# Kernel tuning notes

Measured on AMD Instinct MI355X. Metric: run time of the kernel, lower is better.

## Reference

```python
import jax, jax.numpy as jnp
import numpy as np

KH, KW = 2, 3          # kernel_size of the masked (shifted) conv
CW = KW // 2           # width padding for order 'A'
B, C, H, W = 8, 32, 256, 256
HID = 64


def _wn(v, g):
    # weight normalization: w = g * v / ||v||, norm over (in, kh, kw) per out channel
    norm = jnp.sqrt(jnp.sum(v * v, axis=(1, 2, 3), keepdims=True))
    return v * (g[:, None, None, None] / norm)


def _conv(x, w, b):
    y = jax.lax.conv_general_dilated(
        x, w, window_strides=(1, 1), padding='VALID',
        dimension_numbers=('NCHW', 'OIHW', 'NCHW'))
    return y + b[None, :, None, None]


def setup_inputs() -> dict:
    key = jax.random.key(0)
    ks = jax.random.split(key, 4)
    x = jax.random.normal(ks[0], (B, C, H, W), dtype=jnp.float32)
    v1 = jax.random.normal(ks[1], (HID, C, KH, KW), dtype=jnp.float32) * 0.05
    g1 = jnp.ones((HID,), dtype=jnp.float32)
    b1 = jnp.zeros((HID,), dtype=jnp.float32)
    v2 = jax.random.normal(ks[2], (2 * C, HID, 1, 1), dtype=jnp.float32) * 0.05
    g2 = jnp.ones((2 * C,), dtype=jnp.float32)
    b2 = jnp.zeros((2 * C,), dtype=jnp.float32)
    return {"x": x, "v1": v1, "g1": g1, "b1": b1, "v2": v2, "g2": g2, "b2": b2}


def reference(x, v1, g1, b1, v2, g2, b2):
    # ShiftedConv2d, order 'A': pad KH rows on top, CW cols each side, drop last
    # row, then VALID conv -> output at row h only sees input rows h-KH..h-1.
    xs = jnp.pad(x, ((0, 0), (0, 0), (KH, 0), (CW, CW)))[:, :, :-1, :]
    h = _conv(xs, _wn(v1, g1), b1)                 # [B, HID, H, W]
    h = jax.nn.elu(h)
    ms = _conv(h, _wn(v2, g2), b2)                 # [B, 2C, H, W]
    mu, log_scale = jnp.split(ms, 2, axis=1)
    scale = jax.nn.sigmoid(log_scale + 2.0)
    out = x * scale + mu                           # affine flow
    logdet = jnp.sum(jnp.log(scale).reshape(x.shape[0], -1), axis=1)  # [B]
    return out, logdet
```

## Files before the change

kernel.cpp:

```cpp
#include <hip/hip_runtime.h>
#include <hip/hip_bf16.h>
#include <math.h>

#define B_   8
#define C_   32
#define H_   256
#define W_   256
#define NPIX (B_*C_*H_*W_)

#define PW    260
#define ROWDW (PW*16)
#define ROWB  (ROWDW*4)

typedef __attribute__((ext_vector_type(8))) short short8;
typedef __attribute__((ext_vector_type(4))) float f32x4;
typedef __attribute__((ext_vector_type(2))) float f32x2;

static __device__ __forceinline__ short f2bf(float f) {
    union { __hip_bfloat16 h; short s; } u; u.h = __float2bfloat16(f); return u.s;
}
static __device__ __forceinline__ int cvtpk(float lo, float hi) {
    int r;
    asm("v_cvt_pk_bf16_f32 %0, %1, %2" : "=v"(r) : "v"(lo), "v"(hi));
    return r;
}

__global__ __launch_bounds__(64) void prep_kernel(
    const float* __restrict__ v1, const float* __restrict__ g1,
    const float* __restrict__ v2, const float* __restrict__ g2,
    short* __restrict__ w1b, short* __restrict__ w2b)
{
    const int t   = threadIdx.x;
    const int bid = blockIdx.x;
    if (bid < 64) {
        const int o = bid;
        float a0 = v1[o*192 + t];
        float a1 = v1[o*192 + t + 64];
        float a2 = v1[o*192 + t + 128];
        float s  = a0*a0 + a1*a1 + a2*a2;
        #pragma unroll
        for (int m = 32; m >= 1; m >>= 1) s += __shfl_xor(s, m, 64);
        const float inv = g1[o] / sqrtf(s);
        const int e0 = t, e1 = t + 64, e2 = t + 128;
        w1b[o*192 + (e0%6)*32 + e0/6] = f2bf(a0*inv);
        w1b[o*192 + (e1%6)*32 + e1/6] = f2bf(a1*inv);
        w1b[o*192 + (e2%6)*32 + e2/6] = f2bf(a2*inv);
    } else {
        const int j = bid - 64;
        float a = v2[j*64 + t];
        float s = a*a;
        #pragma unroll
        for (int m = 32; m >= 1; m >>= 1) s += __shfl_xor(s, m, 64);
        const float inv = g2[j] / sqrtf(s);
        const int mt = t >> 4, r = t & 15;
        const int slot = (mt >> 1)*32 + ((r >> 2) << 3) + ((mt & 1) << 2) + (r & 3);
        w2b[j*64 + slot] = f2bf(a*inv);
    }
}

__global__ __launch_bounds__(256) void flow_kernel(
    const float* __restrict__ x,
    const short* __restrict__ w1b, const short* __restrict__ w2b,
    const float* __restrict__ b1,  const float* __restrict__ b2,
    float* __restrict__ out, float* __restrict__ ldpart)
{
    __shared__ int ldsI[2*ROWDW];

    const int bi0 = blockIdx.x;
    const int bi  = (bi0 & 7) * 256 + (bi0 >> 3);
    const int b   = bi >> 8;
    const int h   = bi & 255;

    const int tid  = threadIdx.x;
    const int l    = tid & 63;
    const int wv   = tid >> 6;
    const int lrow = l & 15;
    const int q    = l >> 4;

    const float* xb = x + (size_t)b * (C_*H_*W_);
    float* ob       = out + (size_t)b * (C_*H_*W_);

    {
        const int r   = tid >> 7;
        const int hr  = h - 2 + r;
        const int u   = tid & 127;
        const int w0  = u << 1;
        const int p0  = w0 + 1, p1 = w0 + 2;
        const int sw0 = (p0 >> 2) & 3, sw1 = (p1 >> 2) & 3;
        if (hr >= 0) {
            const float* pr = xb + (size_t)hr * W_ + w0;
            #pragma unroll
            for (int g = 0; g < 4; ++g) {
                f32x2 a[8];
                #pragma unroll
                for (int j = 0; j < 8; ++j)
                    a[j] = *(const f32x2*)(pr + (size_t)(8*g + j) * (H_*W_));
                int4 d0, d1;
                d0.x = cvtpk(a[0][0], a[1][0]); d0.y = cvtpk(a[2][0], a[3][0]);
                d0.z = cvtpk(a[4][0], a[5][0]); d0.w = cvtpk(a[6][0], a[7][0]);
                d1.x = cvtpk(a[0][1], a[1][1]); d1.y = cvtpk(a[2][1], a[3][1]);
                d1.z = cvtpk(a[4][1], a[5][1]); d1.w = cvtpk(a[6][1], a[7][1]);
                *(int4*)&ldsI[r*ROWDW + p0*16 + ((g ^ sw0) << 2)] = d0;
                *(int4*)&ldsI[r*ROWDW + p1*16 + ((g ^ sw1) << 2)] = d1;
            }
        } else {
            const int4 z4 = {0,0,0,0};
            #pragma unroll
            for (int g = 0; g < 4; ++g) {
                *(int4*)&ldsI[r*ROWDW + p0*16 + ((g ^ sw0) << 2)] = z4;
                *(int4*)&ldsI[r*ROWDW + p1*16 + ((g ^ sw1) << 2)] = z4;
            }
        }
        if (tid < 16) {
            const int rz = tid >> 3;
            const int pz = ((tid >> 2) & 1) ? 257 : 0;
            *(int4*)&ldsI[rz*ROWDW + pz*16 + ((tid & 3) << 2)] = (int4){0,0,0,0};
        }
    }
    __syncthreads();

    f32x4 acc1[4][4];
    #pragma unroll
    for (int mt = 0; mt < 4; ++mt) {
        const f32x4 bv = *(const f32x4*)(b1 + mt*16 + 4*q);
        #pragma unroll
        for (int nt = 0; nt < 4; ++nt) acc1[mt][nt] = bv;
    }

    #pragma unroll
    for (int tap = 0; tap < 6; ++tap) {
        const int rb = (tap < 3) ? 0 : ROWB;
        const int dw = (tap % 3) - 1;
        short8 wf[4];
        #pragma unroll
        for (int mt = 0; mt < 4; ++mt)
            wf[mt] = *(const short8*)(w1b + (mt*16 + lrow)*192 + tap*32 + q*8);
        #pragma unroll
        for (int nt = 0; nt < 4; ++nt) {
            const int p = wv*64 + nt*16 + lrow + dw + 1;
            const int byteoff = rb + p*64 + ((q ^ ((p >> 2) & 3)) << 4);
            const short8 xf = *(const short8*)((const char*)ldsI + byteoff);
            #pragma unroll
            for (int mt = 0; mt < 4; ++mt)
                acc1[mt][nt] = __builtin_amdgcn_mfma_f32_16x16x32_bf16(
                                   wf[mt], xf, acc1[mt][nt], 0, 0, 0);
        }
    }

    #pragma unroll
    for (int mt = 0; mt < 4; ++mt)
        #pragma unroll
        for (int nt = 0; nt < 4; ++nt)
            #pragma unroll
            for (int rg = 0; rg < 4; ++rg) {
                const float v = acc1[mt][nt][rg];
                acc1[mt][nt][rg] = v > 0.f ? v : (__expf(v) - 1.f);
            }

    short8 a2f[2][4];
    #pragma unroll
    for (int kt = 0; kt < 2; ++kt)
        #pragma unroll
        for (int mt2 = 0; mt2 < 4; ++mt2)
            a2f[kt][mt2] = *(const short8*)(w2b + (mt2*16 + lrow)*64 + kt*32 + q*8);

    f32x4 acc2[4][4];
    #pragma unroll
    for (int nt = 0; nt < 4; ++nt) {
        union { int4 i; short8 s; } u0, u1;
        u0.i.x = cvtpk(acc1[0][nt][0], acc1[0][nt][1]);
        u0.i.y = cvtpk(acc1[0][nt][2], acc1[0][nt][3]);
        u0.i.z = cvtpk(acc1[1][nt][0], acc1[1][nt][1]);
        u0.i.w = cvtpk(acc1[1][nt][2], acc1[1][nt][3]);
        u1.i.x = cvtpk(acc1[2][nt][0], acc1[2][nt][1]);
        u1.i.y = cvtpk(acc1[2][nt][2], acc1[2][nt][3]);
        u1.i.z = cvtpk(acc1[3][nt][0], acc1[3][nt][1]);
        u1.i.w = cvtpk(acc1[3][nt][2], acc1[3][nt][3]);
        #pragma unroll
        for (int mt2 = 0; mt2 < 4; ++mt2) {
            f32x4 t0 = __builtin_amdgcn_mfma_f32_16x16x32_bf16(
                           a2f[0][mt2], u0.s, (f32x4){0.f,0.f,0.f,0.f}, 0, 0, 0);
            acc2[mt2][nt] = __builtin_amdgcn_mfma_f32_16x16x32_bf16(
                           a2f[1][mt2], u1.s, t0, 0, 0, 0);
        }
    }

    f32x4 b2m[2], b2s[2];
    #pragma unroll
    for (int mt2 = 0; mt2 < 2; ++mt2) {
        b2m[mt2] = *(const f32x4*)(b2 + mt2*16 + 4*q);
        b2s[mt2] = *(const f32x4*)(b2 + 32 + mt2*16 + 4*q);
    }

    float ldsum = 0.f;
    #pragma unroll
    for (int nt = 0; nt < 4; ++nt) {
        const int px = wv*64 + nt*16 + lrow;
        const int colbase = h*W_ + px;
        float pr8 = 1.f;
        #pragma unroll
        for (int mt2 = 0; mt2 < 2; ++mt2)
            #pragma unroll
            for (int rg = 0; rg < 4; ++rg) {
                const float mu = acc2[mt2][nt][rg]     + b2m[mt2][rg];
                const float z  = acc2[mt2 + 2][nt][rg] + b2s[mt2][rg] + 2.f;
                const float sc = 1.f / (1.f + __expf(-z));
                pr8 *= sc;
                const int j = mt2*16 + 4*q + rg;
                const size_t idx = (size_t)j * (H_*W_) + colbase;
                ob[idx] = xb[idx] * sc + mu;
            }
        ldsum += __logf(pr8);
    }

    #pragma unroll
    for (int m = 32; m >= 1; m >>= 1) ldsum += __shfl_xor(ldsum, m, 64);
    if (l == 0) ldpart[(size_t)bi * 4 + wv] = ldsum;
}

__global__ __launch_bounds__(256) void reduce_kernel(
    const float* __restrict__ ldpart, float* __restrict__ logdet)
{
    __shared__ float r4[4];
    const int b = blockIdx.x;
    const int t = threadIdx.x;
    const f32x4 v = *(const f32x4*)(ldpart + (size_t)b*1024 + t*4);
    float s = v[0] + v[1] + v[2] + v[3];
    #pragma unroll
    for (int m = 32; m >= 1; m >>= 1) s += __shfl_xor(s, m, 64);
    if ((t & 63) == 0) r4[t >> 6] = s;
    __syncthreads();
    if (t == 0) logdet[b] = r4[0] + r4[1] + r4[2] + r4[3];
}

extern "C" void kernel_launch(void* const* d_in, const int* in_sizes, int n_in,
                              void* d_out, int out_size, void* d_ws, size_t ws_size,
                              hipStream_t stream)
{
    const float* x  = (const float*)d_in[0];
    const float* v1 = (const float*)d_in[1];
    const float* g1 = (const float*)d_in[2];
    const float* b1 = (const float*)d_in[3];
    const float* v2 = (const float*)d_in[4];
    const float* g2 = (const float*)d_in[5];
    const float* b2 = (const float*)d_in[6];

    float* out    = (float*)d_out;
    float* logdet = out + NPIX;

    short* w1b    = (short*)d_ws;
    short* w2b    = w1b + 12288;
    float* ldpart = (float*)((char*)d_ws + 32768);

    prep_kernel<<<128, 64, 0, stream>>>(v1, g1, v2, g2, w1b, w2b);
    flow_kernel<<<B_ * H_, 256, 0, stream>>>(x, w1b, w2b, b1, b2, out, ldpart);
    reduce_kernel<<<B_, 256, 0, stream>>>(ldpart, logdet);
}
```

Before: 65.22 us.

## Split each image row across two 128-thread blocks with halo loading

```diff
diff --git a/kernel.cpp b/kernel.cpp
--- a/kernel.cpp
+++ b/kernel.cpp
@@ -6,11 +6,12 @@
 #define C_   32
 #define H_   256
 #define W_   256
+#define HW_  (H_*W_)
 #define NPIX (B_*C_*H_*W_)
 
-#define PW    260
-#define ROWDW (PW*16)
-#define ROWB  (ROWDW*4)
+#define SLOTS3  132
+#define ROWDW3  (SLOTS3*16)
+#define ROWB3   (ROWDW3*4)
 
 typedef __attribute__((ext_vector_type(8))) short short8;
 typedef __attribute__((ext_vector_type(4))) float f32x4;
@@ -58,18 +59,19 @@
     }
 }
 
-__global__ __launch_bounds__(256) void flow_kernel(
+__global__ __launch_bounds__(128) void flow_kernel(
     const float* __restrict__ x,
     const short* __restrict__ w1b, const short* __restrict__ w2b,
     const float* __restrict__ b1,  const float* __restrict__ b2,
     float* __restrict__ out, float* __restrict__ ldpart)
 {
-    __shared__ int ldsI[2*ROWDW];
-
-    const int bi0 = blockIdx.x;
-    const int bi  = (bi0 & 7) * 256 + (bi0 >> 3);
-    const int b   = bi >> 8;
-    const int h   = bi & 255;
+    __shared__ int ldsI[2*ROWDW3];
+
+    const int bi0  = blockIdx.x;
+    const int b    = bi0 & 7;
+    const int rest = bi0 >> 3;
+    const int h    = rest >> 1;
+    const int pxb  = (rest & 1) << 7;
 
     const int tid  = threadIdx.x;
     const int l    = tid & 63;
@@ -77,44 +79,53 @@
     const int lrow = l & 15;
     const int q    = l >> 4;
 
-    const float* xb = x + (size_t)b * (C_*H_*W_);
-    float* ob       = out + (size_t)b * (C_*H_*W_);
+    const float* xb = x + (size_t)b * (C_*HW_);
+    float* ob       = out + (size_t)b * (C_*HW_);
 
     {
-        const int r   = tid >> 7;
+        const int r   = tid >> 6;
         const int hr  = h - 2 + r;
-        const int u   = tid & 127;
-        const int w0  = u << 1;
-        const int p0  = w0 + 1, p1 = w0 + 2;
+        const int k   = tid & 63;
+        const int p0  = 2*k + 1, p1 = 2*k + 2;
         const int sw0 = (p0 >> 2) & 3, sw1 = (p1 >> 2) & 3;
         if (hr >= 0) {
-            const float* pr = xb + (size_t)hr * W_ + w0;
+            const float* pr = xb + (size_t)hr * W_ + (pxb + 2*k);
             #pragma unroll
             for (int g = 0; g < 4; ++g) {
                 f32x2 a[8];
                 #pragma unroll
                 for (int j = 0; j < 8; ++j)
-                    a[j] = *(const f32x2*)(pr + (size_t)(8*g + j) * (H_*W_));
+                    a[j] = *(const f32x2*)(pr + (size_t)(8*g + j) * HW_);
                 int4 d0, d1;
                 d0.x = cvtpk(a[0][0], a[1][0]); d0.y = cvtpk(a[2][0], a[3][0]);
                 d0.z = cvtpk(a[4][0], a[5][0]); d0.w = cvtpk(a[6][0], a[7][0]);
                 d1.x = cvtpk(a[0][1], a[1][1]); d1.y = cvtpk(a[2][1], a[3][1]);
                 d1.z = cvtpk(a[4][1], a[5][1]); d1.w = cvtpk(a[6][1], a[7][1]);
-                *(int4*)&ldsI[r*ROWDW + p0*16 + ((g ^ sw0) << 2)] = d0;
-                *(int4*)&ldsI[r*ROWDW + p1*16 + ((g ^ sw1) << 2)] = d1;
+                *(int4*)&ldsI[r*ROWDW3 + p0*16 + ((g ^ sw0) << 2)] = d0;
+                *(int4*)&ldsI[r*ROWDW3 + p1*16 + ((g ^ sw1) << 2)] = d1;
             }
         } else {
             const int4 z4 = {0,0,0,0};
             #pragma unroll
             for (int g = 0; g < 4; ++g) {
-                *(int4*)&ldsI[r*ROWDW + p0*16 + ((g ^ sw0) << 2)] = z4;
-                *(int4*)&ldsI[r*ROWDW + p1*16 + ((g ^ sw1) << 2)] = z4;
-            }
-        }
-        if (tid < 16) {
-            const int rz = tid >> 3;
-            const int pz = ((tid >> 2) & 1) ? 257 : 0;
-            *(int4*)&ldsI[rz*ROWDW + pz*16 + ((tid & 3) << 2)] = (int4){0,0,0,0};
+                *(int4*)&ldsI[r*ROWDW3 + p0*16 + ((g ^ sw0) << 2)] = z4;
+                *(int4*)&ldsI[r*ROWDW3 + p1*16 + ((g ^ sw1) << 2)] = z4;
+            }
+        }
+        if (tid < 64) {
+            const int rz = tid >> 5;
+            const int hc = (tid >> 4) & 1;
+            const int c2 = tid & 15;
+            const int wc = hc ? (pxb + 128) : (pxb - 1);
+            const int pz = hc ? 129 : 0;
+            const int hz = h - 2 + rz;
+            int d = 0;
+            if (hz >= 0 && wc >= 0 && wc < W_) {
+                const float a0 = xb[(size_t)(2*c2  )*HW_ + (size_t)hz*W_ + wc];
+                const float a1 = xb[(size_t)(2*c2+1)*HW_ + (size_t)hz*W_ + wc];
+                d = cvtpk(a0, a1);
+            }
+            ldsI[rz*ROWDW3 + pz*16 + c2] = d;
         }
     }
     __syncthreads();
@@ -129,7 +140,7 @@
 
     #pragma unroll
     for (int tap = 0; tap < 6; ++tap) {
-        const int rb = (tap < 3) ? 0 : ROWB;
+        const int rb = (tap < 3) ? 0 : ROWB3;
         const int dw = (tap % 3) - 1;
         short8 wf[4];
         #pragma unroll
@@ -195,7 +206,7 @@
     float ldsum = 0.f;
     #pragma unroll
     for (int nt = 0; nt < 4; ++nt) {
-        const int px = wv*64 + nt*16 + lrow;
+        const int px = pxb + wv*64 + nt*16 + lrow;
         const int colbase = h*W_ + px;
         float pr8 = 1.f;
         #pragma unroll
@@ -207,7 +218,7 @@
                 const float sc = 1.f / (1.f + __expf(-z));
                 pr8 *= sc;
                 const int j = mt2*16 + 4*q + rg;
-                const size_t idx = (size_t)j * (H_*W_) + colbase;
+                const size_t idx = (size_t)j * HW_ + colbase;
                 ob[idx] = xb[idx] * sc + mu;
             }
         ldsum += __logf(pr8);
@@ -215,7 +226,7 @@
 
     #pragma unroll
     for (int m = 32; m >= 1; m >>= 1) ldsum += __shfl_xor(ldsum, m, 64);
-    if (l == 0) ldpart[(size_t)bi * 4 + wv] = ldsum;
+    if (l == 0) ldpart[(size_t)b * 1024 + rest * 2 + wv] = ldsum;
 }
 
 __global__ __launch_bounds__(256) void reduce_kernel(
@@ -253,6 +264,6 @@
     float* ldpart = (float*)((char*)d_ws + 32768);
 
     prep_kernel<<<128, 64, 0, stream>>>(v1, g1, v2, g2, w1b, w2b);
-    flow_kernel<<<B_ * H_, 256, 0, stream>>>(x, w1b, w2b, b1, b2, out, ldpart);
+    flow_kernel<<<B_ * H_ * 2, 128, 0, stream>>>(x, w1b, w2b, b1, b2, out, ldpart);
     reduce_kernel<<<B_, 256, 0, stream>>>(ldpart, logdet);
 }
```

Result: slower. 66.92 us (+2.6%).
